# Kernel optimization log

Hardware: AMD Instinct MI355X
Metric: run time of the kernel (lower is better)

## Reference

```python
import jax, jax.numpy as jnp
import numpy as np

EPS = 1e-7  # keras backend.epsilon()


def _conv_relu(x, w, b):
    # ConvNormRelu with BatchNorm folded into conv bias at inference
    y = jax.lax.conv_general_dilated(x, w, (1, 1), 'SAME',
                                     dimension_numbers=('NHWC', 'HWIO', 'NHWC'))
    return jax.nn.relu(y + b)


def _mlp(x, mw0, mb0, mw1, mb1, mw2, mb2):
    h = jax.nn.relu(x @ mw0 + mb0)
    h = jax.nn.relu(h @ mw1 + mb1)
    return h @ mw2 + mb2


def setup_inputs() -> dict:
    key = jax.random.key(0)
    ks = jax.random.split(key, 20)
    B, HQ = 2, 384
    feats2 = jax.random.normal(ks[0], (B, 192, 192, 64), jnp.float32)
    feats4 = jax.random.normal(ks[1], (B, 96, 96, 96), jnp.float32)
    feats32 = jax.random.normal(ks[2], (B, 24, 24, 160), jnp.float32)
    coords = jax.random.uniform(ks[3], (B, HQ, HQ, 2), jnp.float32, -1.0, 1.0)
    cells = jnp.full((B, HQ, HQ, 2), 2.0 / HQ, jnp.float32)
    s = 0.05
    params = dict(
        w2=jax.random.normal(ks[4], (1, 1, 64, 32)) * s, b2=jnp.zeros((32,)),
        w4=jax.random.normal(ks[5], (1, 1, 96, 32)) * s, b4=jnp.zeros((32,)),
        w32=jax.random.normal(ks[6], (1, 1, 160, 32)) * s, b32=jnp.zeros((32,)),
        wf=jax.random.normal(ks[7], (3, 3, 96, 96)) * s, bf=jnp.zeros((96,)),
        mw0=jax.random.normal(ks[8], (102, 64)) * s, mb0=jnp.zeros((64,)),
        mw1=jax.random.normal(ks[9], (64, 64)) * s, mb1=jnp.zeros((64,)),
        mw2=jax.random.normal(ks[10], (64, 1)) * s, mb2=jnp.zeros((1,)),
    )
    return dict(feats2=feats2, feats4=feats4, feats32=feats32,
                coords=coords, cells=cells, **params)


def reference(feats2, feats4, feats32, coords, cells,
              w2, b2, w4, b4, w32, b32, wf, bf,
              mw0, mb0, mw1, mb1, mw2, mb2):
    a2 = _conv_relu(feats2, w2, b2)
    a4 = _conv_relu(feats4, w4, b4)
    a32 = _conv_relu(feats32, w32, b32)
    B, H, W, _ = a2.shape
    # resize_by_sample: bilinear upsample to feats2 grid (half-pixel centers)
    a4 = jax.image.resize(a4, (B, H, W, a4.shape[-1]), method='bilinear')
    a32 = jax.image.resize(a32, (B, H, W, a32.shape[-1]), method='bilinear')
    aspp = _conv_relu(jnp.concatenate([a2, a4, a32], axis=-1), wf, bf)

    size = jnp.array([H, W], jnp.float32)
    rxry = 1.0 / size
    rel_cells = cells * size
    bi = jnp.arange(B)[:, None, None]  # batch gather index

    preds, areas = [], []
    for vy in (-1.0, 1.0):  # itertools.product([-1,1],[-1,1]) order
        for vx in (-1.0, 1.0):
            vv = jnp.array([vy, vx], jnp.float32)
            c = jnp.clip(coords + vv * rxry + EPS, -1.0 + EPS, 1.0 - EPS)
            # original reverses (y,x)->(x,y) for GridSample; index directly instead
            # nearest, align_corners=False: i = round((c+1)*N/2 - 0.5)
            iy = jnp.clip(jnp.round((c[..., 0] + 1.0) * H / 2.0 - 0.5).astype(jnp.int32), 0, H - 1)
            ix = jnp.clip(jnp.round((c[..., 1] + 1.0) * W / 2.0 - 0.5).astype(jnp.int32), 0, W - 1)
            feat_samp = aspp[bi, iy, ix]  # [B,HQ,WQ,96] irregular gather
            # nearest-sampling make_coord == analytic pixel centers of (iy,ix)
            coord_samp = jnp.stack(
                [((iy.astype(jnp.float32) + 0.5) / H) * 2.0 - 1.0,
                 ((ix.astype(jnp.float32) + 0.5) / W) * 2.0 - 1.0], axis=-1)
            rel = (coords - coord_samp) * size
            pred = _mlp(jnp.concatenate([feat_samp, rel, coords, rel_cells], axis=-1),
                        mw0, mb0, mw1, mb1, mw2, mb2)
            preds.append(pred)
            area = jnp.abs(jnp.prod(rel, axis=-1, keepdims=True)) + EPS
            areas.insert(0, area)  # pair each pred with opposite corner's area

    num = preds[0] * areas[0] + preds[1] * areas[1] + preds[2] * areas[2] + preds[3] * areas[3]
    den = areas[0] + areas[1] + areas[2] + areas[3]
    return num / den
```

## Files before the change

kernel.cpp:

```cpp
#include <hip/hip_runtime.h>
#include <math.h>


#define HQ 384
#define HA 192
#define NQ (2 * HQ * HQ)
#define NBS (NQ / 1024)
#define NBKT 288
#define NFLAT (NBKT * NBS)

typedef _Float16 half8  __attribute__((ext_vector_type(8)));
typedef _Float16 half4v __attribute__((ext_vector_type(4)));
typedef float    float4v __attribute__((ext_vector_type(4)));

__device__ __forceinline__ int bucket_id(int q, float cy, float cx) {
    const float LO = -1.0f + 1e-7f, HI = 1.0f - 1e-7f;
    const float RXY = 1.0f / (float)HA;
    float c0 = fminf(fmaxf((cy - RXY) + 1e-7f, LO), HI);
    float c1 = fminf(fmaxf((cx - RXY) + 1e-7f, LO), HI);
    int iy = (int)rintf(((c0 + 1.f) * (float)HA) * 0.5f - 0.5f);
    int ix = (int)rintf(((c1 + 1.f) * (float)HA) * 0.5f - 0.5f);
    iy = min(max(iy, 0), HA - 1);
    ix = min(max(ix, 0), HA - 1);
    int b = q / (HQ * HQ);
    return b * 144 + (iy >> 4) * 12 + (ix >> 4);
}

__launch_bounds__(1024)
__global__ void fused_front(const float* __restrict__ coords,
                            int* __restrict__ cntT,
                            unsigned short* __restrict__ lrank,
                            const float* __restrict__ mw0,
                            const float* __restrict__ mw1,
                            const float* __restrict__ wf,
                            _Float16* __restrict__ fragTab,
                            _Float16* __restrict__ fragTabW,
                            const float* __restrict__ feats4,
                            const float* __restrict__ w4,
                            const float* __restrict__ b4,
                            const float* __restrict__ feats32,
                            const float* __restrict__ w32,
                            const float* __restrict__ b32,
                            float* __restrict__ a4s,
                            float* __restrict__ a32s,
                            const float* __restrict__ feats2,
                            const float* __restrict__ w2,
                            const float* __restrict__ b2,
                            _Float16* __restrict__ xcatH) {
    const int blk = blockIdx.x;
    const int tid = threadIdx.x;

    if (blk < 288) {
        __shared__ int lh[NBKT];
        if (tid < NBKT) lh[tid] = 0;
        __syncthreads();
        const int q = blk * 1024 + tid;
        float cy = coords[(size_t)q * 2 + 0];
        float cx = coords[(size_t)q * 2 + 1];
        int r = atomicAdd(&lh[bucket_id(q, cy, cx)], 1);
        lrank[q] = (unsigned short)r;
        __syncthreads();
        if (tid < NBKT) cntT[tid * NBS + blk] = lh[tid];
    } else if (blk < 300) {
        int t = (blk - 288) * 1024 + tid;
        if (t < 1536) {
            int f = t >> 6, L = t & 63;
            int n_ = L & 15, qd = L >> 4;
            _Float16 vals[8];
            if (f < 16) {
                int kc = f >> 2, nt = f & 3;
#pragma unroll
                for (int j = 0; j < 8; ++j) {
                    int kk = kc * 32 + qd * 8 + j;
                    vals[j] = (_Float16)((kk < 102) ? mw0[kk * 64 + nt * 16 + n_] : 0.f);
                }
            } else {
                int g = f - 16;
                int kc = g >> 2, nt = g & 3;
#pragma unroll
                for (int j = 0; j < 8; ++j) {
                    int s_ = (kc + 2 * (j >> 2)) * 16 + qd * 4 + (j & 3);
                    vals[j] = (_Float16)mw1[s_ * 64 + nt * 16 + n_];
                }
            }
#pragma unroll
            for (int j = 0; j < 8; ++j) fragTab[t * 8 + j] = vals[j];
        } else {
            int tw = t - 1536;
            if (tw < 27 * 6 * 64) {
                int s   = tw / 384;
                int rem = tw - s * 384;
                int nt  = rem >> 6;
                int L   = rem & 63;
                int n_  = L & 15, qd = L >> 4;
                int tap = s / 3, kc = s - tap * 3;
#pragma unroll
                for (int j = 0; j < 8; ++j) {
                    int kch = kc * 32 + qd * 8 + j;
                    fragTabW[tw * 8 + j] =
                        (_Float16)wf[(tap * 96 + kch) * 96 + nt * 16 + n_];
                }
            }
        }
    } else if (blk < 444) {
        int t = (blk - 300) * 1024 + tid;
        int p = t >> 3, cg = t & 7;
        const float4v* xr = (const float4v*)(feats4 + (size_t)p * 96);
        float4v acc = *(const float4v*)(b4 + cg * 4);
#pragma unroll
        for (int i4 = 0; i4 < 24; ++i4) {
            float4v xv = xr[i4];
            const float* wr = w4 + (i4 * 4) * 32 + cg * 4;
#pragma unroll
            for (int j = 0; j < 4; ++j) {
                float4v wv = *(const float4v*)(wr + j * 32);
                acc[0] = fmaf(xv[j], wv[0], acc[0]);
                acc[1] = fmaf(xv[j], wv[1], acc[1]);
                acc[2] = fmaf(xv[j], wv[2], acc[2]);
                acc[3] = fmaf(xv[j], wv[3], acc[3]);
            }
        }
        float4v o = {fmaxf(acc[0], 0.f), fmaxf(acc[1], 0.f),
                     fmaxf(acc[2], 0.f), fmaxf(acc[3], 0.f)};
        *(float4v*)(a4s + (size_t)p * 32 + cg * 4) = o;
    } else if (blk < 453) {
        int t = (blk - 444) * 1024 + tid;
        if (t >= 1152 * 8) return;
        int p = t >> 3, cg = t & 7;
        const float4v* xr = (const float4v*)(feats32 + (size_t)p * 160);
        float4v acc = *(const float4v*)(b32 + cg * 4);
#pragma unroll
        for (int i4 = 0; i4 < 40; ++i4) {
            float4v xv = xr[i4];
            const float* wr = w32 + (i4 * 4) * 32 + cg * 4;
#pragma unroll
            for (int j = 0; j < 4; ++j) {
                float4v wv = *(const float4v*)(wr + j * 32);
                acc[0] = fmaf(xv[j], wv[0], acc[0]);
                acc[1] = fmaf(xv[j], wv[1], acc[1]);
                acc[2] = fmaf(xv[j], wv[2], acc[2]);
                acc[3] = fmaf(xv[j], wv[3], acc[3]);
            }
        }
        float4v o = {fmaxf(acc[0], 0.f), fmaxf(acc[1], 0.f),
                     fmaxf(acc[2], 0.f), fmaxf(acc[3], 0.f)};
        *(float4v*)(a32s + (size_t)p * 32 + cg * 4) = o;
    } else {
        int t = (blk - 453) * 1024 + tid;
        int p = t >> 3, cg = t & 7;
        const float4v* xr = (const float4v*)(feats2 + (size_t)p * 64);
        float4v acc = *(const float4v*)(b2 + cg * 4);
#pragma unroll
        for (int i4 = 0; i4 < 16; ++i4) {
            float4v xv = xr[i4];
            const float* wr = w2 + (i4 * 4) * 32 + cg * 4;
#pragma unroll
            for (int j = 0; j < 4; ++j) {
                float4v wv = *(const float4v*)(wr + j * 32);
                acc[0] = fmaf(xv[j], wv[0], acc[0]);
                acc[1] = fmaf(xv[j], wv[1], acc[1]);
                acc[2] = fmaf(xv[j], wv[2], acc[2]);
                acc[3] = fmaf(xv[j], wv[3], acc[3]);
            }
        }
        half4v h;
        h[0] = (_Float16)fmaxf(acc[0], 0.f);
        h[1] = (_Float16)fmaxf(acc[1], 0.f);
        h[2] = (_Float16)fmaxf(acc[2], 0.f);
        h[3] = (_Float16)fmaxf(acc[3], 0.f);
        *(half4v*)(xcatH + (size_t)p * 96 + cg * 4) = h;
    }
}

__launch_bounds__(1024)
__global__ void fused_mid(const int* __restrict__ cntT,
                          int* __restrict__ scanEx,
                          int* __restrict__ chunkTot,
                          const float* __restrict__ a4s,
                          const float* __restrict__ a32s,
                          _Float16* __restrict__ xcatH) {
    const int blk = blockIdx.x;
    const int t = threadIdx.x;

    if (blk < 81) {
        __shared__ int s[1024];
        const int gi = blk * 1024 + t;
        int v = cntT[gi];
        s[t] = v;
        __syncthreads();
        for (int off = 1; off < 1024; off <<= 1) {
            int x = (t >= off) ? s[t - off] : 0;
            __syncthreads();
            s[t] += x;
            __syncthreads();
        }
        scanEx[gi] = s[t] - v;
        if (t == 1023) chunkTot[blk] = s[t];
        return;
    }

    const int z = (blk < 81 + 576) ? 1 : 2;
    int tt = ((z == 1) ? (blk - 81) : (blk - 657)) * 1024 + t;
    int p = tt >> 3, cg = tt & 7;

    const float* src = (z == 1) ? a4s : a32s;
    const int   S    = (z == 1) ? 96 : 24;
    const float inv  = (z == 1) ? 0.5f : 0.125f;
    const int   coff = (z == 1) ? 32 : 64;

    int x = p % HA;
    int r = p / HA;
    int y = r % HA;
    int b = r / HA;

    float u = ((float)y + 0.5f) * inv - 0.5f;
    float v = ((float)x + 0.5f) * inv - 0.5f;
    float fu = floorf(u), fv = floorf(v);
    float wu = u - fu, wv = v - fv;
    int y0 = (int)fu, x0 = (int)fv;
    int y1 = min(y0 + 1, S - 1);
    int x1 = min(x0 + 1, S - 1);
    y0 = max(y0, 0);
    x0 = max(x0, 0);

    const float* sb = src + (size_t)b * S * S * 32 + cg * 4;
    float4v v00 = *(const float4v*)(sb + (y0 * S + x0) * 32);
    float4v v01 = *(const float4v*)(sb + (y0 * S + x1) * 32);
    float4v v10 = *(const float4v*)(sb + (y1 * S + x0) * 32);
    float4v v11 = *(const float4v*)(sb + (y1 * S + x1) * 32);
    half4v h;
#pragma unroll
    for (int j = 0; j < 4; ++j) {
        float t0 = v00[j] * (1.f - wu) + v10[j] * wu;
        float t1 = v01[j] * (1.f - wu) + v11[j] * wu;
        h[j] = (_Float16)(t0 * (1.f - wv) + t1 * wv);
    }
    *(half4v*)(xcatH + (size_t)p * 96 + coff + cg * 4) = h;
}

__launch_bounds__(256, 4)
__global__ void fused_back(const _Float16* __restrict__ xH,
                           const _Float16* __restrict__ fragTabW,
                           const float* __restrict__ bias,
                           _Float16* __restrict__ yH,
                           const float* __restrict__ coords,
                           const float* __restrict__ cells,
                           const int* __restrict__ scanEx,
                           const int* __restrict__ chunkTot,
                           const unsigned short* __restrict__ lrank,
                           int* __restrict__ qidx,
                           float4v* __restrict__ qdata) {
    __shared__ __align__(16) unsigned char smemU[37440];
    const int blk = blockIdx.x;
    const int tid = threadIdx.x;

    if (blk < 576) {
        _Float16* lds = (_Float16*)smemU;
        const int lane = tid & 63;
        const int wv   = tid >> 6;
        const int n_   = lane & 15;
        const int qd   = lane >> 4;
        const int nh   = wv & 1;
        const int yg   = wv >> 1;
        const int bx0  = (blk % 12) * 16;
        const int by0  = ((blk / 12) % 24) * 8;
        const int b    = blk / 288;

        for (int idx = tid; idx < 2160; idx += 256) {
            int hy  = idx / 216;
            int rem = idx - hy * 216;
            int hx  = rem / 12;
            int cc  = rem - hx * 12;
            int gy = by0 + hy - 1, gx = bx0 + hx - 1;
            half8 v = {(_Float16)0.f, (_Float16)0.f, (_Float16)0.f, (_Float16)0.f,
                       (_Float16)0.f, (_Float16)0.f, (_Float16)0.f, (_Float16)0.f};
            if (gy >= 0 && gy < HA && gx >= 0 && gx < HA)
                v = *(const half8*)(xH + (((size_t)b * HA + gy) * HA + gx) * 96 + cc * 8);
            *(half8*)&lds[(hy * 18 + hx) * 104 + cc * 8] = v;
        }

        float bv[3];
#pragma unroll
        for (int j = 0; j < 3; ++j) bv[j] = bias[(nh * 3 + j) * 16 + n_];

        __syncthreads();

        float4v acc[4][3];
#pragma unroll
        for (int r = 0; r < 4; ++r)
#pragma unroll
            for (int j = 0; j < 3; ++j) {
                float4v z = {0.f, 0.f, 0.f, 0.f};
                acc[r][j] = z;
            }

#pragma unroll 1
        for (int ky = 0; ky < 3; ++ky)
#pragma unroll 1
            for (int kx = 0; kx < 3; ++kx) {
                const int tap = ky * 3 + kx;
#pragma unroll
                for (int kc = 0; kc < 3; ++kc) {
                    const int s = tap * 3 + kc;
                    half8 bf[3];
#pragma unroll
                    for (int j = 0; j < 3; ++j)
                        bf[j] = *(const half8*)(fragTabW +
                                ((size_t)(s * 6 + nh * 3 + j) * 64 + lane) * 8);
#pragma unroll
                    for (int r = 0; r < 4; ++r) {
                        const int yr = yg * 4 + r;
                        half8 a = *(const half8*)&lds[((yr + ky) * 18 + (n_ + kx)) * 104
                                                      + kc * 32 + qd * 8];
#pragma unroll
                        for (int j = 0; j < 3; ++j)
                            acc[r][j] = __builtin_amdgcn_mfma_f32_16x16x32_f16(
                                a, bf[j], acc[r][j], 0, 0, 0);
                    }
                }
            }

#pragma unroll
        for (int r = 0; r < 4; ++r) {
            const int gy = by0 + yg * 4 + r;
#pragma unroll
            for (int j = 0; j < 3; ++j) {
                const int ch = (nh * 3 + j) * 16 + n_;
#pragma unroll
                for (int reg = 0; reg < 4; ++reg) {
                    const int gx = bx0 + qd * 4 + reg;
                    yH[(((size_t)b * HA + gy) * HA + gx) * 96 + ch] =
                        (_Float16)fmaxf(acc[r][j][reg] + bv[j], 0.f);
                }
            }
        }
    } else {
        int* pEx = (int*)smemU;
        int v = 0;
        if (tid < 81) v = chunkTot[tid];
        if (tid < 128) pEx[tid] = v;
        __syncthreads();
        for (int off = 1; off < 128; off <<= 1) {
            int x = 0;
            if (tid < 128 && tid >= off) x = pEx[tid - off];
            __syncthreads();
            if (tid < 128) pEx[tid] += x;
            __syncthreads();
        }
        if (tid < 128) pEx[tid] -= v;
        __syncthreads();

        const int q = (blk - 576) * 256 + tid;
        float cy = coords[(size_t)q * 2 + 0];
        float cx = coords[(size_t)q * 2 + 1];
        int bkt = bucket_id(q, cy, cx);
        int sb  = q >> 10;
        int li  = bkt * NBS + sb;
        int pos = pEx[li >> 10] + scanEx[li] + (int)lrank[q];
        qidx[pos] = q;
        float4v d = {cy, cx,
                     cells[(size_t)q * 2 + 0] * (float)HA,
                     cells[(size_t)q * 2 + 1] * (float)HA};
        qdata[pos] = d;
    }
}

__launch_bounds__(1024, 8)
__global__ void decoder_mlp_mfma(const _Float16* __restrict__ asppH,
                                 const int* __restrict__ qidx,
                                 const float4v* __restrict__ qdata,
                                 const _Float16* __restrict__ fragTab,
                                 const float* __restrict__ mb0,
                                 const float* __restrict__ mb1,
                                 const float* __restrict__ mw2,
                                 const float* __restrict__ mb2,
                                 float* __restrict__ out) {
    __shared__ __align__(16) _Float16 fragL[24 * 64 * 8];
    __shared__ __align__(16) float biasL[196];

    const int tid  = threadIdx.x;
    const int lane = tid & 63;
    const int wv   = tid >> 6;
    const int n_   = lane & 15;
    const int qd   = lane >> 4;
    const int R    = (blockIdx.x & 7) * 576 + (blockIdx.x >> 3);

    const int sp = R * 64 + wv * 4 + (n_ >> 2);
    const float4v d = qdata[sp];
    const int   qq = qidx[sp];
    const int   b  = qq / (HQ * HQ);
    const float cy = d[0], cx = d[1], rcy = d[2], rcx = d[3];
    const int   k  = n_ & 3;

    const float LO = -1.0f + 1e-7f, HI = 1.0f - 1e-7f;
    const float RXY = 1.0f / (float)HA;
    const float vy = (k < 2) ? -1.f : 1.f;
    const float vx = (k & 1) ? 1.f : -1.f;

    float c0 = fminf(fmaxf((cy + vy * RXY) + 1e-7f, LO), HI);
    float c1 = fminf(fmaxf((cx + vx * RXY) + 1e-7f, LO), HI);
    int iy = (int)rintf(((c0 + 1.f) * (float)HA) * 0.5f - 0.5f);
    int ix = (int)rintf(((c1 + 1.f) * (float)HA) * 0.5f - 0.5f);
    iy = min(max(iy, 0), HA - 1);
    ix = min(max(ix, 0), HA - 1);

    const float cs0 = (((float)iy + 0.5f) / (float)HA) * 2.f - 1.f;
    const float cs1 = (((float)ix + 0.5f) / (float)HA) * 2.f - 1.f;
    const float r0 = (cy - cs0) * (float)HA;
    const float r1 = (cx - cs1) * (float)HA;
    const float area = fabsf(r0 * r1) + 1e-7f;
    const int   pix = ((b * HA + iy) * HA + ix) * 96;

    half8 A_[4];
    A_[0] = *(const half8*)(asppH + pix + 0 * 32 + qd * 8);
    A_[1] = *(const half8*)(asppH + pix + 1 * 32 + qd * 8);
    A_[2] = *(const half8*)(asppH + pix + 2 * 32 + qd * 8);
    {
        half8 e = {(_Float16)0.f, (_Float16)0.f, (_Float16)0.f, (_Float16)0.f,
                   (_Float16)0.f, (_Float16)0.f, (_Float16)0.f, (_Float16)0.f};
        if (qd == 0) {
            e[0] = (_Float16)r0;  e[1] = (_Float16)r1;
            e[2] = (_Float16)cy;  e[3] = (_Float16)cx;
            e[4] = (_Float16)rcy; e[5] = (_Float16)rcx;
        }
        A_[3] = e;
    }

#pragma unroll
    for (int it = 0; it < 2; ++it) {
        const int i = it * 1024 + tid;
        if (i < 1536)
            *(half8*)&fragL[i * 8] = *(const half8*)(fragTab + (size_t)i * 8);
    }
    if (tid < 64) {
        biasL[tid]       = mb0[tid];
        biasL[64 + tid]  = mb1[tid];
        biasL[128 + tid] = mw2[tid];
    }
    if (tid == 0) biasL[192] = mb2[0];
    __syncthreads();

    float4v acc[4];
#pragma unroll
    for (int nt = 0; nt < 4; ++nt)
        acc[nt] = *(const float4v*)&biasL[nt * 16 + qd * 4];
#pragma unroll
    for (int kc = 0; kc < 4; ++kc)
#pragma unroll
        for (int nt = 0; nt < 4; ++nt) {
            half8 w0 = *(const half8*)&fragL[((kc * 4 + nt) * 64 + lane) * 8];
            acc[nt] = __builtin_amdgcn_mfma_f32_16x16x32_f16(w0, A_[kc],
                                                             acc[nt], 0, 0, 0);
        }

    half8 b1[2];
#pragma unroll
    for (int kc = 0; kc < 2; ++kc) {
        half8 t;
#pragma unroll
        for (int j = 0; j < 4; ++j) {
            t[j]     = (_Float16)fmaxf(acc[kc][j], 0.f);
            t[j + 4] = (_Float16)fmaxf(acc[kc + 2][j], 0.f);
        }
        b1[kc] = t;
    }

    float4v acc1[4];
#pragma unroll
    for (int nt = 0; nt < 4; ++nt)
        acc1[nt] = *(const float4v*)&biasL[64 + nt * 16 + qd * 4];
#pragma unroll
    for (int kc = 0; kc < 2; ++kc)
#pragma unroll
        for (int nt = 0; nt < 4; ++nt) {
            half8 w1 = *(const half8*)&fragL[((16 + kc * 4 + nt) * 64 + lane) * 8];
            acc1[nt] = __builtin_amdgcn_mfma_f32_16x16x32_f16(w1, b1[kc],
                                                              acc1[nt], 0, 0, 0);
        }

    float s = 0.f;
#pragma unroll
    for (int nt = 0; nt < 4; ++nt) {
        float4v w2q = *(const float4v*)&biasL[128 + nt * 16 + qd * 4];
#pragma unroll
        for (int reg = 0; reg < 4; ++reg)
            s = fmaf(fmaxf(acc1[nt][reg], 0.f), w2q[reg], s);
    }
    s += __shfl_xor(s, 16, 64);
    s += __shfl_xor(s, 32, 64);
    const float p = s + biasL[192];

    float a_opp = __shfl_xor(area, 3, 64);
    float np = p * a_opp;
    float dp = area;
    np += __shfl_xor(np, 1, 64);
    dp += __shfl_xor(dp, 1, 64);
    np += __shfl_xor(np, 2, 64);
    dp += __shfl_xor(dp, 2, 64);

    if ((lane & 0x33) == 0)
        out[qq] = np / dp;
}

extern "C" void kernel_launch(void* const* d_in, const int* in_sizes, int n_in,
                              void* d_out, int out_size, void* d_ws, size_t ws_size,
                              hipStream_t stream) {
    (void)in_sizes; (void)n_in; (void)out_size; (void)ws_size;
    const float* feats2  = (const float*)d_in[0];
    const float* feats4  = (const float*)d_in[1];
    const float* feats32 = (const float*)d_in[2];
    const float* coords  = (const float*)d_in[3];
    const float* cells   = (const float*)d_in[4];
    const float* w2  = (const float*)d_in[5];
    const float* b2  = (const float*)d_in[6];
    const float* w4  = (const float*)d_in[7];
    const float* b4  = (const float*)d_in[8];
    const float* w32 = (const float*)d_in[9];
    const float* b32 = (const float*)d_in[10];
    const float* wf  = (const float*)d_in[11];
    const float* bf  = (const float*)d_in[12];
    const float* mw0 = (const float*)d_in[13];
    const float* mb0 = (const float*)d_in[14];
    const float* mw1 = (const float*)d_in[15];
    const float* mb1 = (const float*)d_in[16];
    const float* mw2 = (const float*)d_in[17];
    const float* mb2 = (const float*)d_in[18];

    float* ws = (float*)d_ws;
    float*    a4s   = ws;
    float*    a32s  = a4s + 589824;
    _Float16* xcatH = (_Float16*)(a32s + 36864);
    _Float16* asppH = xcatH + 7077888;
    _Float16* fragTab  = asppH + 7077888;
    _Float16* fragTabW = fragTab + 12288;
    float4v*  qdata = (float4v*)(fragTabW + 82944);
    int*      qidx  = (int*)(qdata + NQ);
    int*      cntT  = qidx + NQ;
    int*      scanEx = cntT + NFLAT;
    int*      chunkTot = scanEx + NFLAT;
    unsigned short* lrank = (unsigned short*)(chunkTot + 128);
    float* out = (float*)d_out;

    fused_front<<<1029, 1024, 0, stream>>>(coords, cntT, lrank,
                                           mw0, mw1, wf, fragTab, fragTabW,
                                           feats4, w4, b4, feats32, w32, b32,
                                           a4s, a32s, feats2, w2, b2, xcatH);
    fused_mid<<<1233, 1024, 0, stream>>>(cntT, scanEx, chunkTot,
                                         a4s, a32s, xcatH);
    fused_back<<<1728, 256, 0, stream>>>(xcatH, fragTabW, bf, asppH,
                                         coords, cells, scanEx, chunkTot,
                                         lrank, qidx, qdata);
    decoder_mlp_mfma<<<4608, 1024, 0, stream>>>(asppH, qidx, qdata, fragTab,
                                                mb0, mb1, mw2, mb2, out);
}
```

Measured before the change: 204.2 us.

## Switch decoder MLP to 32x32x16 MFMA with biases folded into weights

Rewrites the decoder MLP to use 32x32x16 f16 MFMA tiles covering 32 sample-corner columns per wave instead of 16x16x32 tiles, so each block handles twice as many queries and the grid is halved. The layer-0 and layer-1 biases are folded into the packed weight fragments as an extra K row multiplied by a constant 1 input, which removes the bias initialisation loads from shared memory. The K dimension is padded differently (7 steps for layer 0, 5 for layer 1), adding some zero-padded MFMA work, and the register footprint per lane grows with the larger accumulators.

```diff
diff --git a/kernel.cpp b/kernel.cpp
--- a/kernel.cpp
+++ b/kernel.cpp
@@ -12,6 +12,7 @@
 typedef _Float16 half8  __attribute__((ext_vector_type(8)));
 typedef _Float16 half4v __attribute__((ext_vector_type(4)));
 typedef float    float4v __attribute__((ext_vector_type(4)));
+typedef float    float16v __attribute__((ext_vector_type(16)));
 
 __device__ __forceinline__ int bucket_id(int q, float cy, float cx) {
     const float LO = -1.0f + 1e-7f, HI = 1.0f - 1e-7f;
@@ -31,7 +32,9 @@
                             int* __restrict__ cntT,
                             unsigned short* __restrict__ lrank,
                             const float* __restrict__ mw0,
+                            const float* __restrict__ mb0f,
                             const float* __restrict__ mw1,
+                            const float* __restrict__ mb1f,
                             const float* __restrict__ wf,
                             _Float16* __restrict__ fragTab,
                             _Float16* __restrict__ fragTabW,
@@ -65,22 +68,33 @@
         int t = (blk - 288) * 1024 + tid;
         if (t < 1536) {
             int f = t >> 6, L = t & 63;
-            int n_ = L & 15, qd = L >> 4;
+            int h = L >> 5;
             _Float16 vals[8];
-            if (f < 16) {
-                int kc = f >> 2, nt = f & 3;
+            if (f < 14) {
+                int ks = f >> 1, nt = f & 1;
+                int col = nt * 32 + (L & 31);
 #pragma unroll
                 for (int j = 0; j < 8; ++j) {
-                    int kk = kc * 32 + qd * 8 + j;
-                    vals[j] = (_Float16)((kk < 102) ? mw0[kk * 64 + nt * 16 + n_] : 0.f);
+                    int kk = ks * 16 + h * 8 + j;
+                    float v = (kk < 102) ? mw0[kk * 64 + col]
+                            : ((kk == 102) ? mb0f[col] : 0.f);
+                    vals[j] = (_Float16)v;
                 }
             } else {
-                int g = f - 16;
-                int kc = g >> 2, nt = g & 3;
+                int g = f - 14;
+                int ks = g >> 1, nt = g & 1;
+                int col = nt * 32 + (L & 31);
 #pragma unroll
                 for (int j = 0; j < 8; ++j) {
-                    int s_ = (kc + 2 * (j >> 2)) * 16 + qd * 4 + (j & 3);
-                    vals[j] = (_Float16)mw1[s_ * 64 + nt * 16 + n_];
+                    int kp = ks * 16 + h * 8 + j;
+                    float v;
+                    if (ks < 4) {
+                        int n = (kp & 0x33) | ((kp & 8) >> 1) | ((kp & 4) << 1);
+                        v = mw1[n * 64 + col];
+                    } else {
+                        v = (kp == 64) ? mb1f[col] : 0.f;
+                    }
+                    vals[j] = (_Float16)v;
                 }
             }
 #pragma unroll
@@ -370,27 +384,25 @@
                                  const int* __restrict__ qidx,
                                  const float4v* __restrict__ qdata,
                                  const _Float16* __restrict__ fragTab,
-                                 const float* __restrict__ mb0,
-                                 const float* __restrict__ mb1,
                                  const float* __restrict__ mw2,
                                  const float* __restrict__ mb2,
                                  float* __restrict__ out) {
     __shared__ __align__(16) _Float16 fragL[24 * 64 * 8];
-    __shared__ __align__(16) float biasL[196];
+    __shared__ __align__(16) float biasL[68];
 
     const int tid  = threadIdx.x;
     const int lane = tid & 63;
     const int wv   = tid >> 6;
-    const int n_   = lane & 15;
-    const int qd   = lane >> 4;
-    const int R    = (blockIdx.x & 7) * 576 + (blockIdx.x >> 3);
-
-    const int sp = R * 64 + wv * 4 + (n_ >> 2);
+    const int h    = lane >> 5;
+    const int col  = lane & 31;
+    const int R    = (blockIdx.x & 7) * 288 + (blockIdx.x >> 3);
+
+    const int sp = R * 128 + wv * 8 + (col >> 2);
     const float4v d = qdata[sp];
     const int   qq = qidx[sp];
     const int   b  = qq / (HQ * HQ);
     const float cy = d[0], cx = d[1], rcy = d[2], rcx = d[3];
-    const int   k  = n_ & 3;
+    const int   k  = col & 3;
 
     const float LO = -1.0f + 1e-7f, HI = 1.0f - 1e-7f;
     const float RXY = 1.0f / (float)HA;
@@ -411,20 +423,10 @@
     const float area = fabsf(r0 * r1) + 1e-7f;
     const int   pix = ((b * HA + iy) * HA + ix) * 96;
 
-    half8 A_[4];
-    A_[0] = *(const half8*)(asppH + pix + 0 * 32 + qd * 8);
-    A_[1] = *(const half8*)(asppH + pix + 1 * 32 + qd * 8);
-    A_[2] = *(const half8*)(asppH + pix + 2 * 32 + qd * 8);
-    {
-        half8 e = {(_Float16)0.f, (_Float16)0.f, (_Float16)0.f, (_Float16)0.f,
-                   (_Float16)0.f, (_Float16)0.f, (_Float16)0.f, (_Float16)0.f};
-        if (qd == 0) {
-            e[0] = (_Float16)r0;  e[1] = (_Float16)r1;
-            e[2] = (_Float16)cy;  e[3] = (_Float16)cx;
-            e[4] = (_Float16)rcy; e[5] = (_Float16)rcx;
-        }
-        A_[3] = e;
-    }
+    half8 Xf[3];
+    Xf[0] = *(const half8*)(asppH + pix + 0 * 16 + h * 8);
+    Xf[1] = *(const half8*)(asppH + pix + 1 * 16 + h * 8);
+    Xf[2] = *(const half8*)(asppH + pix + 2 * 16 + h * 8);
 
 #pragma unroll
     for (int it = 0; it < 2; ++it) {
@@ -432,63 +434,96 @@
         if (i < 1536)
             *(half8*)&fragL[i * 8] = *(const half8*)(fragTab + (size_t)i * 8);
     }
-    if (tid < 64) {
-        biasL[tid]       = mb0[tid];
-        biasL[64 + tid]  = mb1[tid];
-        biasL[128 + tid] = mw2[tid];
-    }
-    if (tid == 0) biasL[192] = mb2[0];
+    if (tid < 64) biasL[tid] = mw2[tid];
+    if (tid == 0) biasL[64] = mb2[0];
     __syncthreads();
 
-    float4v acc[4];
-#pragma unroll
-    for (int nt = 0; nt < 4; ++nt)
-        acc[nt] = *(const float4v*)&biasL[nt * 16 + qd * 4];
-#pragma unroll
-    for (int kc = 0; kc < 4; ++kc)
-#pragma unroll
-        for (int nt = 0; nt < 4; ++nt) {
-            half8 w0 = *(const half8*)&fragL[((kc * 4 + nt) * 64 + lane) * 8];
-            acc[nt] = __builtin_amdgcn_mfma_f32_16x16x32_f16(w0, A_[kc],
+    float16v acc[2];
+    {
+        float16v z{};
+        acc[0] = z;
+        acc[1] = z;
+    }
+#pragma unroll
+    for (int ks = 0; ks < 3; ++ks)
+#pragma unroll
+        for (int nt = 0; nt < 2; ++nt) {
+            half8 w0 = *(const half8*)&fragL[((ks * 2 + nt) * 64 + lane) * 8];
+            acc[nt] = __builtin_amdgcn_mfma_f32_32x32x16_f16(w0, Xf[ks],
                                                              acc[nt], 0, 0, 0);
         }
 
-    half8 b1[2];
-#pragma unroll
-    for (int kc = 0; kc < 2; ++kc) {
+    Xf[0] = *(const half8*)(asppH + pix + 3 * 16 + h * 8);
+    Xf[1] = *(const half8*)(asppH + pix + 4 * 16 + h * 8);
+    Xf[2] = *(const half8*)(asppH + pix + 5 * 16 + h * 8);
+#pragma unroll
+    for (int ks = 0; ks < 3; ++ks)
+#pragma unroll
+        for (int nt = 0; nt < 2; ++nt) {
+            half8 w0 = *(const half8*)&fragL[(((ks + 3) * 2 + nt) * 64 + lane) * 8];
+            acc[nt] = __builtin_amdgcn_mfma_f32_32x32x16_f16(w0, Xf[ks],
+                                                             acc[nt], 0, 0, 0);
+        }
+    {
+        half8 e = {(_Float16)0.f, (_Float16)0.f, (_Float16)0.f, (_Float16)0.f,
+                   (_Float16)0.f, (_Float16)0.f, (_Float16)0.f, (_Float16)0.f};
+        if (h == 0) {
+            e[0] = (_Float16)r0;  e[1] = (_Float16)r1;
+            e[2] = (_Float16)cy;  e[3] = (_Float16)cx;
+            e[4] = (_Float16)rcy; e[5] = (_Float16)rcx;
+            e[6] = (_Float16)1.f;
+        }
+#pragma unroll
+        for (int nt = 0; nt < 2; ++nt) {
+            half8 w0 = *(const half8*)&fragL[((6 * 2 + nt) * 64 + lane) * 8];
+            acc[nt] = __builtin_amdgcn_mfma_f32_32x32x16_f16(w0, e,
+                                                             acc[nt], 0, 0, 0);
+        }
+    }
+
+    half8 b1f[5];
+#pragma unroll
+    for (int ks = 0; ks < 4; ++ks) {
         half8 t;
 #pragma unroll
-        for (int j = 0; j < 4; ++j) {
-            t[j]     = (_Float16)fmaxf(acc[kc][j], 0.f);
-            t[j + 4] = (_Float16)fmaxf(acc[kc + 2][j], 0.f);
-        }
-        b1[kc] = t;
-    }
-
-    float4v acc1[4];
-#pragma unroll
-    for (int nt = 0; nt < 4; ++nt)
-        acc1[nt] = *(const float4v*)&biasL[64 + nt * 16 + qd * 4];
-#pragma unroll
-    for (int kc = 0; kc < 2; ++kc)
-#pragma unroll
-        for (int nt = 0; nt < 4; ++nt) {
-            half8 w1 = *(const half8*)&fragL[((16 + kc * 4 + nt) * 64 + lane) * 8];
-            acc1[nt] = __builtin_amdgcn_mfma_f32_16x16x32_f16(w1, b1[kc],
+        for (int j = 0; j < 8; ++j)
+            t[j] = (_Float16)fmaxf(acc[ks >> 1][(ks & 1) * 8 + j], 0.f);
+        b1f[ks] = t;
+    }
+    {
+        half8 e = {(_Float16)0.f, (_Float16)0.f, (_Float16)0.f, (_Float16)0.f,
+                   (_Float16)0.f, (_Float16)0.f, (_Float16)0.f, (_Float16)0.f};
+        if (h == 0) e[0] = (_Float16)1.f;
+        b1f[4] = e;
+    }
+
+    float16v acc1[2];
+    {
+        float16v z{};
+        acc1[0] = z;
+        acc1[1] = z;
+    }
+#pragma unroll
+    for (int ks = 0; ks < 5; ++ks)
+#pragma unroll
+        for (int nt = 0; nt < 2; ++nt) {
+            half8 w1 = *(const half8*)&fragL[(((14 + ks * 2 + nt)) * 64 + lane) * 8];
+            acc1[nt] = __builtin_amdgcn_mfma_f32_32x32x16_f16(w1, b1f[ks],
                                                               acc1[nt], 0, 0, 0);
         }
 
     float s = 0.f;
 #pragma unroll
-    for (int nt = 0; nt < 4; ++nt) {
-        float4v w2q = *(const float4v*)&biasL[128 + nt * 16 + qd * 4];
-#pragma unroll
-        for (int reg = 0; reg < 4; ++reg)
-            s = fmaf(fmaxf(acc1[nt][reg], 0.f), w2q[reg], s);
-    }
-    s += __shfl_xor(s, 16, 64);
+    for (int nt = 0; nt < 2; ++nt)
+#pragma unroll
+        for (int q = 0; q < 4; ++q) {
+            float4v w2v = *(const float4v*)&biasL[nt * 32 + q * 8 + h * 4];
+#pragma unroll
+            for (int i = 0; i < 4; ++i)
+                s = fmaf(fmaxf(acc1[nt][q * 4 + i], 0.f), w2v[i], s);
+        }
     s += __shfl_xor(s, 32, 64);
-    const float p = s + biasL[192];
+    const float p = s + biasL[64];
 
     float a_opp = __shfl_xor(area, 3, 64);
     float np = p * a_opp;
@@ -498,7 +533,7 @@
     np += __shfl_xor(np, 2, 64);
     dp += __shfl_xor(dp, 2, 64);
 
-    if ((lane & 0x33) == 0)
+    if ((lane & 0x23) == 0)
         out[qq] = np / dp;
 }
 
@@ -542,7 +577,8 @@
     float* out = (float*)d_out;
 
     fused_front<<<1029, 1024, 0, stream>>>(coords, cntT, lrank,
-                                           mw0, mw1, wf, fragTab, fragTabW,
+                                           mw0, mb0, mw1, mb1, wf,
+                                           fragTab, fragTabW,
                                            feats4, w4, b4, feats32, w32, b32,
                                            a4s, a32s, feats2, w2, b2, xcatH);
     fused_mid<<<1233, 1024, 0, stream>>>(cntT, scanEx, chunkTot,
@@ -550,6 +586,6 @@
     fused_back<<<1728, 256, 0, stream>>>(xcatH, fragTabW, bf, asppH,
                                          coords, cells, scanEx, chunkTot,
                                          lrank, qidx, qdata);
-    decoder_mlp_mfma<<<4608, 1024, 0, stream>>>(asppH, qidx, qdata, fragTab,
-                                                mb0, mb1, mw2, mb2, out);
+    decoder_mlp_mfma<<<2304, 1024, 0, stream>>>(asppH, qidx, qdata, fragTab,
+                                                mw2, mb2, out);
 }
```

After: 193.1 us (median of 3 runs). 5.4% less time.
